# Kernel tuning notes

Measured on AMD Instinct MI355X. Metric: run time of the kernel, lower is better.

Reference implementation:

```python
import jax, jax.numpy as jnp
import numpy as np

B, T, C = 4, 2048, 1024
H, D = 16, 64  # n_heads, head_dim; C == H*D

def setup_inputs() -> dict:
    key = jax.random.key(0)
    ks = jax.random.split(key, 6)
    s_in = 1.0 / np.sqrt(C)
    x = jax.random.normal(ks[0], (B, T, C), dtype=jnp.float32)
    # causal mask: True above the diagonal -> masked to -inf
    mask = jnp.triu(jnp.ones((T, T), dtype=bool), k=1)
    Wqkv = jax.random.uniform(ks[1], (C, 3 * C), jnp.float32, -s_in, s_in)
    bqkv = jax.random.uniform(ks[2], (3 * C,), jnp.float32, -s_in, s_in)
    Wout = jax.random.uniform(ks[3], (C, C), jnp.float32, -s_in, s_in)
    bout = jax.random.uniform(ks[4], (C,), jnp.float32, -s_in, s_in)
    return {"x": x, "mask": mask, "Wqkv": Wqkv, "bqkv": bqkv, "Wout": Wout, "bout": bout}

def reference(x, mask, Wqkv, bqkv, Wout, bout):
    b, t, c = x.shape
    qkv = (x @ Wqkv + bqkv).reshape(b, t, 3, H, D)
    qkv = jnp.transpose(qkv, (2, 0, 3, 1, 4))  # [3, B, H, T, D]
    q, k, v = qkv[0], qkv[1], qkv[2]
    scores = jnp.einsum("bhqd,bhkd->bhqk", q, k) / jnp.sqrt(jnp.float32(D))
    scores = jnp.where(mask[:t, :t][None, None, :, :], -jnp.inf, scores)
    attn = jax.nn.softmax(scores, axis=-1)
    out = jnp.einsum("bhqk,bhkd->bhqd", attn, v)
    out = jnp.transpose(out, (0, 2, 1, 3)).reshape(b, t, c)
    return out @ Wout + bout
```

## Files before the change

### kernel.cpp

```cpp
#include <hip/hip_runtime.h>

typedef unsigned short u16;
typedef __attribute__((ext_vector_type(8))) short bf16x8;
typedef __attribute__((ext_vector_type(4))) short bf16x4;
typedef __attribute__((ext_vector_type(4))) float f32x4;

#define MFMA16(a, b, c) __builtin_amdgcn_mfma_f32_16x16x32_bf16(a, b, c, 0, 0, 0)

__device__ __forceinline__ u16 f2bf(float x) {
    unsigned u = __float_as_uint(x);
    return (u16)((u + 0x7fffu + ((u >> 16) & 1u)) >> 16);
}
__device__ __forceinline__ u16 f2bf_fast(float x) {
    return (u16)((__float_as_uint(x) + 0x8000u) >> 16);
}

__global__ __launch_bounds__(256) void castk(const float* __restrict__ src, u16* __restrict__ dst) {
    const int i = (blockIdx.x * 256 + threadIdx.x) * 8;
    float4 a = *(const float4*)(src + i);
    float4 b = *(const float4*)(src + i + 4);
    bf16x8 v;
    v[0] = (short)f2bf(a.x); v[1] = (short)f2bf(a.y);
    v[2] = (short)f2bf(a.z); v[3] = (short)f2bf(a.w);
    v[4] = (short)f2bf(b.x); v[5] = (short)f2bf(b.y);
    v[6] = (short)f2bf(b.z); v[7] = (short)f2bf(b.w);
    *(bf16x8*)(dst + i) = v;
}

__global__ __launch_bounds__(256) void tkern(const float* __restrict__ src, u16* __restrict__ dst,
                                             int R, int C) {
    const int tC = C >> 6;
    const int tr = (blockIdx.x / tC) << 6;
    const int tc = (blockIdx.x % tC) << 6;
    __shared__ u16 ls[64 * 68];
    const int tid = threadIdx.x;
#pragma unroll
    for (int rep = 0; rep < 2; ++rep) {
        const int f = tid * 8 + rep * 2048;
        const int r = f >> 6, c = f & 63;
        float4 a = *(const float4*)(src + (size_t)(tr + r) * C + tc + c);
        float4 b = *(const float4*)(src + (size_t)(tr + r) * C + tc + c + 4);
        bf16x4 lo, hi;
        lo[0] = (short)f2bf(a.x); lo[1] = (short)f2bf(a.y);
        lo[2] = (short)f2bf(a.z); lo[3] = (short)f2bf(a.w);
        hi[0] = (short)f2bf(b.x); hi[1] = (short)f2bf(b.y);
        hi[2] = (short)f2bf(b.z); hi[3] = (short)f2bf(b.w);
        *(bf16x4*)&ls[r * 68 + c] = lo;
        *(bf16x4*)&ls[r * 68 + c + 4] = hi;
    }
    __syncthreads();
#pragma unroll
    for (int rep = 0; rep < 2; ++rep) {
        const int f = tid * 8 + rep * 2048;
        const int rn = f >> 6, ck = f & 63;
        bf16x8 v;
#pragma unroll
        for (int j = 0; j < 8; ++j) v[j] = (short)ls[(ck + j) * 68 + rn];
        *(bf16x8*)(dst + (size_t)(tc + rn) * R + tr + ck) = v;
    }
}

template <int MODE>
__global__ __launch_bounds__(256) void gemm_k(const u16* __restrict__ A, const u16* __restrict__ Bt,
                                              const float* __restrict__ bias,
                                              u16* __restrict__ Qo, u16* __restrict__ Ko,
                                              u16* __restrict__ Vo, float* __restrict__ Of) {
    constexpr int Kd = 1024;
    const int tid = threadIdx.x;
    const int lane = tid & 63, wave = tid >> 6;
    const int wm = wave >> 1, wn = wave & 1;
    const int lr = lane & 15, lg = lane >> 4;
    const int mt = blockIdx.x & 63;
    const int nt = blockIdx.x >> 6;
    const int mbase = mt << 7, nbase = nt << 7;
    __shared__ u16 As[128 * 32];
    __shared__ u16 Bs[128 * 32];
    f32x4 acc[4][4];
#pragma unroll
    for (int i = 0; i < 4; ++i)
#pragma unroll
        for (int j = 0; j < 4; ++j) acc[i][j] = {0.f, 0.f, 0.f, 0.f};

    for (int kb = 0; kb < Kd; kb += 32) {
        __syncthreads();
#pragma unroll
        for (int rep = 0; rep < 2; ++rep) {
            const int f = tid * 8 + rep * 2048;
            const int r = f >> 5, c = f & 31;
            __builtin_amdgcn_global_load_lds(
                (const __attribute__((address_space(1))) void*)(A + (size_t)(mbase + r) * Kd + kb + c),
                (__attribute__((address_space(3))) void*)(As + f), 16, 0, 0);
            __builtin_amdgcn_global_load_lds(
                (const __attribute__((address_space(1))) void*)(Bt + (size_t)(nbase + r) * Kd + kb + c),
                (__attribute__((address_space(3))) void*)(Bs + f), 16, 0, 0);
        }
        __syncthreads();
        bf16x8 af[4], bfr[4];
#pragma unroll
        for (int i = 0; i < 4; ++i)
            af[i] = *(const bf16x8*)&As[(wm * 64 + i * 16 + lr) * 32 + lg * 8];
#pragma unroll
        for (int j = 0; j < 4; ++j)
            bfr[j] = *(const bf16x8*)&Bs[(wn * 64 + j * 16 + lr) * 32 + lg * 8];
#pragma unroll
        for (int i = 0; i < 4; ++i)
#pragma unroll
            for (int j = 0; j < 4; ++j) acc[i][j] = MFMA16(af[i], bfr[j], acc[i][j]);
    }

    const float QSCALE = 0.1803368801111137f;
#pragma unroll
    for (int j = 0; j < 4; ++j) {
        const int n = nbase + wn * 64 + j * 16 + lr;
        const float bj = bias[n];
        if (MODE == 0) {
            const int three = n >> 10;
            const int h = (n >> 6) & 15;
            const int d = n & 63;
#pragma unroll
            for (int i = 0; i < 4; ++i) {
#pragma unroll
                for (int r = 0; r < 4; ++r) {
                    const int m = mbase + wm * 64 + i * 16 + lg * 4 + r;
                    const int b = m >> 11, t = m & 2047;
                    const int bh = (b << 4) + h;
                    const float val = acc[i][j][r] + bj;
                    if (three == 0)
                        Qo[(((size_t)bh << 11) + t) * 64 + d] = f2bf(val * QSCALE);
                    else if (three == 1)
                        Ko[(((size_t)bh << 11) + t) * 64 + d] = f2bf(val);
                    else
                        Vo[(((size_t)bh << 6) + d) * 2048 + t] = f2bf(val);
                }
            }
        } else {
#pragma unroll
            for (int i = 0; i < 4; ++i) {
#pragma unroll
                for (int r = 0; r < 4; ++r) {
                    const int m = mbase + wm * 64 + i * 16 + lg * 4 + r;
                    Of[((size_t)m << 10) + n] = acc[i][j][r] + bj;
                }
            }
        }
    }
}

__global__ __launch_bounds__(256) void flash_attn(const u16* __restrict__ Q, const u16* __restrict__ Kg,
                                                  const u16* __restrict__ Vt, u16* __restrict__ Aout) {
    const int tid = threadIdx.x;
    const int lane = tid & 63, wave = tid >> 6;
    const int lr = lane & 15, lg = lane >> 4;
    const int bid = blockIdx.x;
    const int swz = (bid & 7) * 128 + (bid >> 3);
    const int bh = swz >> 4;
    const int bx = swz & 15;
    const int b = bh >> 4, h = bh & 15;
    const size_t base = (size_t)bh << 17;

    const int qb_hi = 16 + bx;
    const int qb_lo = 15 - bx;

    __shared__ u16 Ks[2][64 * 64];
    __shared__ u16 Vs[2][64 * 64];
    __shared__ u16 Ps[4][16 * 64];

    int qbase[2];
    qbase[0] = qb_hi * 64 + wave * 16;
    qbase[1] = qb_lo * 64 + wave * 16;

    bf16x8 qf[2][2];
#pragma unroll
    for (int st = 0; st < 2; ++st) {
        const u16* p = Q + base + (size_t)(qbase[st] + lr) * 64;
        qf[st][0] = *(const bf16x8*)(p + lg * 8);
        qf[st][1] = *(const bf16x8*)(p + 32 + lg * 8);
    }

    f32x4 o[2][4];
#pragma unroll
    for (int st = 0; st < 2; ++st)
#pragma unroll
        for (int dt = 0; dt < 4; ++dt) o[st][dt] = {0.f, 0.f, 0.f, 0.f};
    float m_[2] = {-INFINITY, -INFINITY};
    float l_[2] = {0.f, 0.f};

    const int f0 = tid * 16;
    const int row0 = f0 >> 7, c0 = (f0 >> 4) & 7;
    const int cc0 = c0 ^ (row0 & 7);
    const int f1 = (tid + 256) * 16;
    const int row1 = f1 >> 7, c1 = (f1 >> 4) & 7;
    const int cc1 = c1 ^ (row1 & 7);

    const int xr = lr & 7;

    auto stage = [&](int sel, int kt) {
        const size_t krow = base + (size_t)(kt * 64) * 64;
        __builtin_amdgcn_global_load_lds(
            (const __attribute__((address_space(1))) void*)(Kg + krow + (size_t)row0 * 64 + cc0 * 8),
            (__attribute__((address_space(3))) void*)(&Ks[sel][tid * 8]), 16, 0, 0);
        __builtin_amdgcn_global_load_lds(
            (const __attribute__((address_space(1))) void*)(Kg + krow + (size_t)row1 * 64 + cc1 * 8),
            (__attribute__((address_space(3))) void*)(&Ks[sel][2048 + tid * 8]), 16, 0, 0);
        __builtin_amdgcn_global_load_lds(
            (const __attribute__((address_space(1))) void*)(Vt + base + (size_t)row0 * 2048 + kt * 64 + cc0 * 8),
            (__attribute__((address_space(3))) void*)(&Vs[sel][tid * 8]), 16, 0, 0);
        __builtin_amdgcn_global_load_lds(
            (const __attribute__((address_space(1))) void*)(Vt + base + (size_t)row1 * 2048 + kt * 64 + cc1 * 8),
            (__attribute__((address_space(3))) void*)(&Vs[sel][2048 + tid * 8]), 16, 0, 0);
    };

    auto process = [&](int sel, int st, bool diag, int kt) {
        f32x4 s[4];
#pragma unroll
        for (int rt = 0; rt < 4; ++rt) {
            const int krow = rt * 16 + lr;
            const bf16x8 k0 = *(const bf16x8*)&Ks[sel][krow * 64 + ((lg) ^ xr) * 8];
            const bf16x8 k1 = *(const bf16x8*)&Ks[sel][krow * 64 + ((lg + 4) ^ xr) * 8];
            f32x4 z = {0.f, 0.f, 0.f, 0.f};
            z = MFMA16(k0, qf[st][0], z);
            z = MFMA16(k1, qf[st][1], z);
            s[rt] = z;
        }
        if (diag) {
            const int q_glob = qbase[st] + lr;
#pragma unroll
            for (int rt = 0; rt < 4; ++rt)
#pragma unroll
                for (int r = 0; r < 4; ++r) {
                    const int kv = kt * 64 + rt * 16 + lg * 4 + r;
                    if (kv > q_glob) s[rt][r] = -INFINITY;
                }
        }
        float rmax = -INFINITY;
#pragma unroll
        for (int rt = 0; rt < 4; ++rt)
#pragma unroll
            for (int r = 0; r < 4; ++r) rmax = fmaxf(rmax, s[rt][r]);
        rmax = fmaxf(rmax, __shfl_xor(rmax, 16));
        rmax = fmaxf(rmax, __shfl_xor(rmax, 32));
        const float m_new = fmaxf(m_[st], rmax);
        const float alpha = exp2f(m_[st] - m_new);
        float rsum = 0.f;
#pragma unroll
        for (int rt = 0; rt < 4; ++rt)
#pragma unroll
            for (int r = 0; r < 4; ++r) {
                const float p = exp2f(s[rt][r] - m_new);
                s[rt][r] = p;
                rsum += p;
            }
        rsum += __shfl_xor(rsum, 16);
        rsum += __shfl_xor(rsum, 32);
        l_[st] = l_[st] * alpha + rsum;
        m_[st] = m_new;

        u16* psb = &Ps[wave][0];
#pragma unroll
        for (int rt = 0; rt < 4; ++rt) {
            bf16x4 pk;
#pragma unroll
            for (int r = 0; r < 4; ++r) pk[r] = (short)f2bf_fast(s[rt][r]);
            *(bf16x4*)&psb[lr * 64 + (((rt * 2 + (lg >> 1)) ^ xr) << 3) + ((lg & 1) << 2)] = pk;
        }
        float aq[4];
#pragma unroll
        for (int r = 0; r < 4; ++r) aq[r] = __shfl(alpha, (lane & 48) + lg * 4 + r);
#pragma unroll
        for (int dt = 0; dt < 4; ++dt)
#pragma unroll
            for (int r = 0; r < 4; ++r) o[st][dt][r] *= aq[r];

        const bf16x8 pf0 = *(const bf16x8*)&psb[lr * 64 + ((lg ^ xr) << 3)];
        const bf16x8 pf1 = *(const bf16x8*)&psb[lr * 64 + (((4 + lg) ^ xr) << 3)];
#pragma unroll
        for (int dt = 0; dt < 4; ++dt) {
            const int vrow = dt * 16 + lr;
            const bf16x8 v0 = *(const bf16x8*)&Vs[sel][vrow * 64 + ((lg) ^ xr) * 8];
            const bf16x8 v1 = *(const bf16x8*)&Vs[sel][vrow * 64 + ((lg + 4) ^ xr) * 8];
            o[st][dt] = MFMA16(pf0, v0, o[st][dt]);
            o[st][dt] = MFMA16(pf1, v1, o[st][dt]);
        }
    };

    stage(0, 0);
    for (int kt = 0; kt <= qb_hi; ++kt) {
        const int cur = kt & 1;
        __syncthreads();
        if (kt < qb_hi) stage(cur ^ 1, kt + 1);
        process(cur, 0, kt == qb_hi, kt);
        if (kt <= qb_lo) process(cur, 1, kt == qb_lo, kt);
    }

#pragma unroll
    for (int st = 0; st < 2; ++st) {
        const float linv = 1.f / l_[st];
        float lq[4];
#pragma unroll
        for (int r = 0; r < 4; ++r) lq[r] = __shfl(linv, (lane & 48) + lg * 4 + r);
#pragma unroll
        for (int dt = 0; dt < 4; ++dt)
#pragma unroll
            for (int r = 0; r < 4; ++r) {
                const int t = qbase[st] + lg * 4 + r;
                Aout[(((size_t)(b << 11) + t) << 10) + h * 64 + dt * 16 + lr] =
                    f2bf(o[st][dt][r] * lq[r]);
            }
    }
}

extern "C" void kernel_launch(void* const* d_in, const int* in_sizes, int n_in,
                              void* d_out, int out_size, void* d_ws, size_t ws_size,
                              hipStream_t stream) {
    (void)in_sizes; (void)n_in; (void)out_size; (void)ws_size;
    const float* x    = (const float*)d_in[0];
    const float* Wqkv = (const float*)d_in[2];
    const float* bqkv = (const float*)d_in[3];
    const float* Wout = (const float*)d_in[4];
    const float* bout = (const float*)d_in[5];
    float* out = (float*)d_out;

    char* ws = (char*)d_ws;
    u16* WqkvT = (u16*)(ws);
    u16* WoutT = (u16*)(ws + 6291456);
    u16* xb    = (u16*)(ws + 8388608);
    u16* Qb    = (u16*)(ws + 25165824);
    u16* Kb    = (u16*)(ws + 41943040);
    u16* Vtb   = (u16*)(ws + 58720256);
    u16* Ab    = (u16*)(ws + 75497472);

    castk<<<dim3(4096), 256, 0, stream>>>(x, xb);
    tkern<<<dim3(16 * 48), 256, 0, stream>>>(Wqkv, WqkvT, 1024, 3072);
    tkern<<<dim3(16 * 16), 256, 0, stream>>>(Wout, WoutT, 1024, 1024);
    gemm_k<0><<<dim3(64 * 24), 256, 0, stream>>>(xb, WqkvT, bqkv, Qb, Kb, Vtb, nullptr);
    flash_attn<<<dim3(1024), 256, 0, stream>>>(Qb, Kb, Vtb, Ab);
    gemm_k<1><<<dim3(64 * 8), 256, 0, stream>>>(Ab, WoutT, bout, nullptr, nullptr, nullptr, out);
}
```

Before: 320.8 us.

## Interleave both query strips per KV tile and skip rescale when max unchanged

Restructures the attention inner loop so the hi and lo query strips share each K/V fragment load from LDS and their QK and PV MFMAs are interleaved, instead of running two sequential process calls that each reload K and V. It also adds a wave-uniform check that skips the alpha shuffle and accumulator rescale when the running max did not grow, and rewrites the max and sum reductions as trees. Together these aim to cut LDS traffic, expose more independent MFMA work, and trim softmax overhead. In exchange, register pressure rises and the branches are divergent-safe but add control flow.

```diff
diff --git a/kernel.cpp b/kernel.cpp
--- a/kernel.cpp
+++ b/kernel.cpp
@@ -165,25 +165,26 @@
     __shared__ u16 Vs[2][64 * 64];
     __shared__ u16 Ps[4][16 * 64];
 
-    int qbase[2];
-    qbase[0] = qb_hi * 64 + wave * 16;
-    qbase[1] = qb_lo * 64 + wave * 16;
-
-    bf16x8 qf[2][2];
-#pragma unroll
-    for (int st = 0; st < 2; ++st) {
-        const u16* p = Q + base + (size_t)(qbase[st] + lr) * 64;
-        qf[st][0] = *(const bf16x8*)(p + lg * 8);
-        qf[st][1] = *(const bf16x8*)(p + 32 + lg * 8);
-    }
-
-    f32x4 o[2][4];
-#pragma unroll
-    for (int st = 0; st < 2; ++st)
-#pragma unroll
-        for (int dt = 0; dt < 4; ++dt) o[st][dt] = {0.f, 0.f, 0.f, 0.f};
-    float m_[2] = {-INFINITY, -INFINITY};
-    float l_[2] = {0.f, 0.f};
+    const int qbase0 = qb_hi * 64 + wave * 16;
+    const int qbase1 = qb_lo * 64 + wave * 16;
+
+    bf16x8 qf0[2], qf1[2];
+    {
+        const u16* p0 = Q + base + (size_t)(qbase0 + lr) * 64;
+        qf0[0] = *(const bf16x8*)(p0 + lg * 8);
+        qf0[1] = *(const bf16x8*)(p0 + 32 + lg * 8);
+        const u16* p1 = Q + base + (size_t)(qbase1 + lr) * 64;
+        qf1[0] = *(const bf16x8*)(p1 + lg * 8);
+        qf1[1] = *(const bf16x8*)(p1 + 32 + lg * 8);
+    }
+
+    f32x4 o0[4], o1[4];
+#pragma unroll
+    for (int dt = 0; dt < 4; ++dt) {
+        o0[dt] = {0.f, 0.f, 0.f, 0.f};
+        o1[dt] = {0.f, 0.f, 0.f, 0.f};
+    }
+    float m0 = -INFINITY, l0 = 0.f, m1 = -INFINITY, l1 = 0.f;
 
     const int f0 = tid * 16;
     const int row0 = f0 >> 7, c0 = (f0 >> 4) & 7;
@@ -210,50 +211,43 @@
             (__attribute__((address_space(3))) void*)(&Vs[sel][2048 + tid * 8]), 16, 0, 0);
     };
 
-    auto process = [&](int sel, int st, bool diag, int kt) {
-        f32x4 s[4];
-#pragma unroll
-        for (int rt = 0; rt < 4; ++rt) {
-            const int krow = rt * 16 + lr;
-            const bf16x8 k0 = *(const bf16x8*)&Ks[sel][krow * 64 + ((lg) ^ xr) * 8];
-            const bf16x8 k1 = *(const bf16x8*)&Ks[sel][krow * 64 + ((lg + 4) ^ xr) * 8];
-            f32x4 z = {0.f, 0.f, 0.f, 0.f};
-            z = MFMA16(k0, qf[st][0], z);
-            z = MFMA16(k1, qf[st][1], z);
-            s[rt] = z;
-        }
-        if (diag) {
-            const int q_glob = qbase[st] + lr;
-#pragma unroll
-            for (int rt = 0; rt < 4; ++rt)
-#pragma unroll
-                for (int r = 0; r < 4; ++r) {
-                    const int kv = kt * 64 + rt * 16 + lg * 4 + r;
-                    if (kv > q_glob) s[rt][r] = -INFINITY;
-                }
-        }
-        float rmax = -INFINITY;
-#pragma unroll
-        for (int rt = 0; rt < 4; ++rt)
-#pragma unroll
-            for (int r = 0; r < 4; ++r) rmax = fmaxf(rmax, s[rt][r]);
+    auto finish = [&](f32x4 (&s)[4], float& m, float& l, f32x4 (&o)[4],
+                      bf16x8& pfa, bf16x8& pfb) {
+        const float t0 = fmaxf(fmaxf(s[0][0], s[0][1]), s[0][2]);
+        const float t1 = fmaxf(fmaxf(s[0][3], s[1][0]), s[1][1]);
+        const float t2 = fmaxf(fmaxf(s[1][2], s[1][3]), s[2][0]);
+        const float t3 = fmaxf(fmaxf(s[2][1], s[2][2]), s[2][3]);
+        const float t4 = fmaxf(fmaxf(s[3][0], s[3][1]), s[3][2]);
+        float rmax = fmaxf(fmaxf(fmaxf(t0, t1), t2), fmaxf(fmaxf(t3, t4), s[3][3]));
         rmax = fmaxf(rmax, __shfl_xor(rmax, 16));
         rmax = fmaxf(rmax, __shfl_xor(rmax, 32));
-        const float m_new = fmaxf(m_[st], rmax);
-        const float alpha = exp2f(m_[st] - m_new);
-        float rsum = 0.f;
+
+        float alpha = 1.f;
+        if (!__all(rmax <= m)) {
+            const float m_new = fmaxf(m, rmax);
+            alpha = exp2f(m - m_new);
+            float aq[4];
+#pragma unroll
+            for (int r = 0; r < 4; ++r) aq[r] = __shfl(alpha, (lane & 48) + lg * 4 + r);
+#pragma unroll
+            for (int dt = 0; dt < 4; ++dt)
+#pragma unroll
+                for (int r = 0; r < 4; ++r) o[dt][r] *= aq[r];
+            m = m_new;
+        }
+
 #pragma unroll
         for (int rt = 0; rt < 4; ++rt)
 #pragma unroll
-            for (int r = 0; r < 4; ++r) {
-                const float p = exp2f(s[rt][r] - m_new);
-                s[rt][r] = p;
-                rsum += p;
-            }
+            for (int r = 0; r < 4; ++r) s[rt][r] = exp2f(s[rt][r] - m);
+        const float u0 = (s[0][0] + s[0][1]) + (s[0][2] + s[0][3]);
+        const float u1 = (s[1][0] + s[1][1]) + (s[1][2] + s[1][3]);
+        const float u2 = (s[2][0] + s[2][1]) + (s[2][2] + s[2][3]);
+        const float u3 = (s[3][0] + s[3][1]) + (s[3][2] + s[3][3]);
+        float rsum = (u0 + u1) + (u2 + u3);
         rsum += __shfl_xor(rsum, 16);
         rsum += __shfl_xor(rsum, 32);
-        l_[st] = l_[st] * alpha + rsum;
-        m_[st] = m_new;
+        l = l * alpha + rsum;
 
         u16* psb = &Ps[wave][0];
 #pragma unroll
@@ -263,24 +257,8 @@
             for (int r = 0; r < 4; ++r) pk[r] = (short)f2bf_fast(s[rt][r]);
             *(bf16x4*)&psb[lr * 64 + (((rt * 2 + (lg >> 1)) ^ xr) << 3) + ((lg & 1) << 2)] = pk;
         }
-        float aq[4];
-#pragma unroll
-        for (int r = 0; r < 4; ++r) aq[r] = __shfl(alpha, (lane & 48) + lg * 4 + r);
-#pragma unroll
-        for (int dt = 0; dt < 4; ++dt)
-#pragma unroll
-            for (int r = 0; r < 4; ++r) o[st][dt][r] *= aq[r];
-
-        const bf16x8 pf0 = *(const bf16x8*)&psb[lr * 64 + ((lg ^ xr) << 3)];
-        const bf16x8 pf1 = *(const bf16x8*)&psb[lr * 64 + (((4 + lg) ^ xr) << 3)];
-#pragma unroll
-        for (int dt = 0; dt < 4; ++dt) {
-            const int vrow = dt * 16 + lr;
-            const bf16x8 v0 = *(const bf16x8*)&Vs[sel][vrow * 64 + ((lg) ^ xr) * 8];
-            const bf16x8 v1 = *(const bf16x8*)&Vs[sel][vrow * 64 + ((lg + 4) ^ xr) * 8];
-            o[st][dt] = MFMA16(pf0, v0, o[st][dt]);
-            o[st][dt] = MFMA16(pf1, v1, o[st][dt]);
-        }
+        pfa = *(const bf16x8*)&psb[lr * 64 + ((lg ^ xr) << 3)];
+        pfb = *(const bf16x8*)&psb[lr * 64 + (((4 + lg) ^ xr) << 3)];
     };
 
     stage(0, 0);
@@ -288,23 +266,87 @@
         const int cur = kt & 1;
         __syncthreads();
         if (kt < qb_hi) stage(cur ^ 1, kt + 1);
-        process(cur, 0, kt == qb_hi, kt);
-        if (kt <= qb_lo) process(cur, 1, kt == qb_lo, kt);
-    }
-
-#pragma unroll
-    for (int st = 0; st < 2; ++st) {
-        const float linv = 1.f / l_[st];
+        const bool do1 = (kt <= qb_lo);
+
+        f32x4 s0[4], s1[4];
+#pragma unroll
+        for (int rt = 0; rt < 4; ++rt) {
+            const int krow = rt * 16 + lr;
+            const bf16x8 k0 = *(const bf16x8*)&Ks[cur][krow * 64 + ((lg) ^ xr) * 8];
+            const bf16x8 k1 = *(const bf16x8*)&Ks[cur][krow * 64 + ((lg + 4) ^ xr) * 8];
+            f32x4 z = {0.f, 0.f, 0.f, 0.f};
+            z = MFMA16(k0, qf0[0], z);
+            z = MFMA16(k1, qf0[1], z);
+            s0[rt] = z;
+            if (do1) {
+                f32x4 w = {0.f, 0.f, 0.f, 0.f};
+                w = MFMA16(k0, qf1[0], w);
+                w = MFMA16(k1, qf1[1], w);
+                s1[rt] = w;
+            }
+        }
+        if (kt == qb_hi) {
+            const int q_glob = qbase0 + lr;
+#pragma unroll
+            for (int rt = 0; rt < 4; ++rt)
+#pragma unroll
+                for (int r = 0; r < 4; ++r) {
+                    const int kv = kt * 64 + rt * 16 + lg * 4 + r;
+                    if (kv > q_glob) s0[rt][r] = -INFINITY;
+                }
+        }
+        if (do1 && kt == qb_lo) {
+            const int q_glob = qbase1 + lr;
+#pragma unroll
+            for (int rt = 0; rt < 4; ++rt)
+#pragma unroll
+                for (int r = 0; r < 4; ++r) {
+                    const int kv = kt * 64 + rt * 16 + lg * 4 + r;
+                    if (kv > q_glob) s1[rt][r] = -INFINITY;
+                }
+        }
+
+        bf16x8 pf00, pf01, pf10, pf11;
+        finish(s0, m0, l0, o0, pf00, pf01);
+        if (do1) finish(s1, m1, l1, o1, pf10, pf11);
+
+#pragma unroll
+        for (int dt = 0; dt < 4; ++dt) {
+            const int vrow = dt * 16 + lr;
+            const bf16x8 v0 = *(const bf16x8*)&Vs[cur][vrow * 64 + ((lg) ^ xr) * 8];
+            const bf16x8 v1 = *(const bf16x8*)&Vs[cur][vrow * 64 + ((lg + 4) ^ xr) * 8];
+            o0[dt] = MFMA16(pf00, v0, o0[dt]);
+            o0[dt] = MFMA16(pf01, v1, o0[dt]);
+            if (do1) {
+                o1[dt] = MFMA16(pf10, v0, o1[dt]);
+                o1[dt] = MFMA16(pf11, v1, o1[dt]);
+            }
+        }
+    }
+
+    {
+        const float linv0 = 1.f / l0;
         float lq[4];
 #pragma unroll
-        for (int r = 0; r < 4; ++r) lq[r] = __shfl(linv, (lane & 48) + lg * 4 + r);
+        for (int r = 0; r < 4; ++r) lq[r] = __shfl(linv0, (lane & 48) + lg * 4 + r);
 #pragma unroll
         for (int dt = 0; dt < 4; ++dt)
 #pragma unroll
             for (int r = 0; r < 4; ++r) {
-                const int t = qbase[st] + lg * 4 + r;
+                const int t = qbase0 + lg * 4 + r;
                 Aout[(((size_t)(b << 11) + t) << 10) + h * 64 + dt * 16 + lr] =
-                    f2bf(o[st][dt][r] * lq[r]);
+                    f2bf(o0[dt][r] * lq[r]);
+            }
+        const float linv1 = 1.f / l1;
+#pragma unroll
+        for (int r = 0; r < 4; ++r) lq[r] = __shfl(linv1, (lane & 48) + lg * 4 + r);
+#pragma unroll
+        for (int dt = 0; dt < 4; ++dt)
+#pragma unroll
+            for (int r = 0; r < 4; ++r) {
+                const int t = qbase1 + lg * 4 + r;
+                Aout[(((size_t)(b << 11) + t) << 10) + h * 64 + dt * 16 + lr] =
+                    f2bf(o1[dt][r] * lq[r]);
             }
     }
 }
```

Result: slower. 342.3 us (+6.7%).

## Remap GEMM tiles per XCD and skip softmax rescale when max unchanged

Applied to the files above, without the earlier changes.

The GEMM block index is remapped so that consecutive M-tiles share an XCD, with the aim of improving L2 reuse of the shared operand tiles. In the attention inner loop, the rescaling of the output accumulator and running sum is skipped when no lane's running max increases (wave-uniform check). The max and sum reductions are rewritten as shallower trees to cut dependency chain length. The skip adds a branch and changes when the row max is updated, but the result stays exact.

```diff
diff --git a/kernel.cpp b/kernel.cpp
--- a/kernel.cpp
+++ b/kernel.cpp
@@ -70,8 +70,11 @@
     const int lane = tid & 63, wave = tid >> 6;
     const int wm = wave >> 1, wn = wave & 1;
     const int lr = lane & 15, lg = lane >> 4;
-    const int mt = blockIdx.x & 63;
-    const int nt = blockIdx.x >> 6;
+    const int bid = blockIdx.x;
+    const int xcd = bid & 7;
+    const int cc = bid >> 3;
+    const int mt = xcd * 8 + (cc & 7);
+    const int nt = cc >> 3;
     const int mbase = mt << 7, nbase = nt << 7;
     __shared__ u16 As[128 * 32];
     __shared__ u16 Bs[128 * 32];
@@ -232,28 +235,41 @@
                     if (kv > q_glob) s[rt][r] = -INFINITY;
                 }
         }
-        float rmax = -INFINITY;
-#pragma unroll
-        for (int rt = 0; rt < 4; ++rt)
-#pragma unroll
-            for (int r = 0; r < 4; ++r) rmax = fmaxf(rmax, s[rt][r]);
+        const float t0 = fmaxf(fmaxf(s[0][0], s[0][1]), s[0][2]);
+        const float t1 = fmaxf(fmaxf(s[0][3], s[1][0]), s[1][1]);
+        const float t2 = fmaxf(fmaxf(s[1][2], s[1][3]), s[2][0]);
+        const float t3 = fmaxf(fmaxf(s[2][1], s[2][2]), s[2][3]);
+        const float t4 = fmaxf(fmaxf(s[3][0], s[3][1]), s[3][2]);
+        float rmax = fmaxf(fmaxf(fmaxf(t0, t1), t2), fmaxf(fmaxf(t3, t4), s[3][3]));
         rmax = fmaxf(rmax, __shfl_xor(rmax, 16));
         rmax = fmaxf(rmax, __shfl_xor(rmax, 32));
-        const float m_new = fmaxf(m_[st], rmax);
-        const float alpha = exp2f(m_[st] - m_new);
-        float rsum = 0.f;
+
+        if (!__all(rmax <= m_[st])) {
+            const float m_new = fmaxf(m_[st], rmax);
+            const float alpha = exp2f(m_[st] - m_new);
+            float aq[4];
+#pragma unroll
+            for (int r = 0; r < 4; ++r) aq[r] = __shfl(alpha, (lane & 48) + lg * 4 + r);
+#pragma unroll
+            for (int dt = 0; dt < 4; ++dt)
+#pragma unroll
+                for (int r = 0; r < 4; ++r) o[st][dt][r] *= aq[r];
+            l_[st] *= alpha;
+            m_[st] = m_new;
+        }
+
 #pragma unroll
         for (int rt = 0; rt < 4; ++rt)
 #pragma unroll
-            for (int r = 0; r < 4; ++r) {
-                const float p = exp2f(s[rt][r] - m_new);
-                s[rt][r] = p;
-                rsum += p;
-            }
+            for (int r = 0; r < 4; ++r) s[rt][r] = exp2f(s[rt][r] - m_[st]);
+        const float u0 = (s[0][0] + s[0][1]) + (s[0][2] + s[0][3]);
+        const float u1 = (s[1][0] + s[1][1]) + (s[1][2] + s[1][3]);
+        const float u2 = (s[2][0] + s[2][1]) + (s[2][2] + s[2][3]);
+        const float u3 = (s[3][0] + s[3][1]) + (s[3][2] + s[3][3]);
+        float rsum = (u0 + u1) + (u2 + u3);
         rsum += __shfl_xor(rsum, 16);
         rsum += __shfl_xor(rsum, 32);
-        l_[st] = l_[st] * alpha + rsum;
-        m_[st] = m_new;
+        l_[st] += rsum;
 
         u16* psb = &Ps[wave][0];
 #pragma unroll
@@ -263,13 +279,6 @@
             for (int r = 0; r < 4; ++r) pk[r] = (short)f2bf_fast(s[rt][r]);
             *(bf16x4*)&psb[lr * 64 + (((rt * 2 + (lg >> 1)) ^ xr) << 3) + ((lg & 1) << 2)] = pk;
         }
-        float aq[4];
-#pragma unroll
-        for (int r = 0; r < 4; ++r) aq[r] = __shfl(alpha, (lane & 48) + lg * 4 + r);
-#pragma unroll
-        for (int dt = 0; dt < 4; ++dt)
-#pragma unroll
-            for (int r = 0; r < 4; ++r) o[st][dt][r] *= aq[r];
 
         const bf16x8 pf0 = *(const bf16x8*)&psb[lr * 64 + ((lg ^ xr) << 3)];
         const bf16x8 pf1 = *(const bf16x8*)&psb[lr * 64 + (((4 + lg) ^ xr) << 3)];
```

Measured after the change: 321.1 us. No clear change (+0.1%).
